# Kernel optimization log

Measured on AMD Instinct MI355X. Metric: run time of the kernel, lower is better.

The kernel has to match this reference:

```python
import jax, jax.numpy as jnp
import numpy as np

N = 100000      # nodes
E = 3200000     # edges (avg degree 32)
DIN, DH, DOUT = 128, 32, 2


def setup_inputs() -> dict:
    key = jax.random.key(0)
    k1, k2, k3, k4 = jax.random.split(key, 4)
    x = jax.random.normal(k1, (N, DIN), dtype=jnp.float32)
    edge_index = jax.random.randint(k2, (2, E), 0, N, dtype=jnp.int64)
    # Glorot-ish scaled weights
    W1 = jax.random.normal(k3, (DIN, DH), dtype=jnp.float32) / np.sqrt(DIN)
    b1 = jnp.zeros((DH,), dtype=jnp.float32)
    W2 = jax.random.normal(k4, (DH, DOUT), dtype=jnp.float32) / np.sqrt(DH)
    b2 = jnp.zeros((DOUT,), dtype=jnp.float32)
    return {"x": x, "edge_index": edge_index, "W1": W1, "b1": b1, "W2": W2, "b2": b2}


def reference(x, edge_index, W1, b1, W2, b2):
    n = x.shape[0]
    # GCNConv default: add self-loops, symmetric deg^{-1/2} A deg^{-1/2} normalization
    loops = jnp.arange(n, dtype=edge_index.dtype)
    src = jnp.concatenate([edge_index[0], loops])  # [E+N]
    dst = jnp.concatenate([edge_index[1], loops])  # [E+N]
    deg = jax.ops.segment_sum(jnp.ones_like(dst, dtype=x.dtype), dst, num_segments=n)
    dinv = jnp.where(deg > 0, jax.lax.rsqrt(deg), 0.0)
    norm = dinv[src] * dinv[dst]  # [E+N]

    def gcn_layer(h, W, b):
        m = h @ W                                   # [n, dout] transform first (PyG order)
        msgs = m[src] * norm[:, None]               # gather + scale  [E+N, dout]
        agg = jax.ops.segment_sum(msgs, dst, num_segments=n)  # scatter-add
        return agg + b

    h = jax.nn.relu(gcn_layer(x, W1, b1))
    return gcn_layer(h, W2, b2)
```

## Files before the change

### kernel.cpp

```cpp
#include <hip/hip_runtime.h>
#include <hip/hip_bf16.h>

#define DIN 128
#define DH 32
#define DOUT 2
#define NPB 128
#define NPB_SHIFT 7
#define NBUK_MAX 1024
#define FILL_EDGES 8192
#define ECHUNK 2048
#define CAP 5632

#define FXS1 2048.0f
#define FXI1 (1.0f / 2048.0f)
#define FXS2 131072.0f
#define FXI2 (1.0f / 131072.0f)


__device__ inline int sxlo(unsigned int w) { return (int)(short)(w & 0xFFFFu); }
__device__ inline int sxhi(unsigned int w) { return ((int)w) >> 16; }

__global__ void zero_kernel(int* __restrict__ gcur, int nbuk,
                            unsigned int* __restrict__ mqrow) {
    int i = blockIdx.x * blockDim.x + threadIdx.x;
    if (i < nbuk) gcur[i] = 0;
    if (blockIdx.x == 0 && threadIdx.x < 16) mqrow[threadIdx.x] = 0u;
}

__global__ void __launch_bounds__(1024, 2)
binfill_kernel(const int* __restrict__ src, const int* __restrict__ dst,
               int* __restrict__ gcur, unsigned int* __restrict__ binned,
               int e, int nbuk) {
    __shared__ int cnt[NBUK_MAX];
    __shared__ int pos[NBUK_MAX];
    __shared__ int gb[NBUK_MAX];
    __shared__ int stmp[1024];
    __shared__ unsigned int sorted[FILL_EDGES];
    __shared__ unsigned short aux[FILL_EDGES];

    int t = threadIdx.x;
    int e0 = blockIdx.x * FILL_EDGES;
    int m = min(FILL_EDGES, e - e0);

    if (t < nbuk) cnt[t] = 0;
    __syncthreads();
    for (int i = t; i < m; i += 1024) atomicAdd(&cnt[dst[e0 + i] >> NPB_SHIFT], 1);
    __syncthreads();

    int v = (t < nbuk) ? cnt[t] : 0;
    stmp[t] = v;
    __syncthreads();
    for (int off = 1; off < 1024; off <<= 1) {
        int x = (t >= off) ? stmp[t - off] : 0;
        __syncthreads();
        stmp[t] += x;
        __syncthreads();
    }
    if (t < nbuk) pos[t] = stmp[t] - v;
    __syncthreads();

    for (int i = t; i < m; i += 1024) {
        int d = dst[e0 + i];
        int sv = src[e0 + i];
        int b = d >> NPB_SHIFT;
        int r = atomicAdd(&pos[b], 1);
        sorted[r] = ((unsigned int)(d & (NPB - 1)) << 17) | (unsigned int)sv;
        aux[r] = (unsigned short)b;
    }
    __syncthreads();

    if (t < nbuk) {
        int c = cnt[t];
        gb[t] = c ? atomicAdd(&gcur[t], c) : 0;
    }
    __syncthreads();

    for (int i = t; i < m; i += 1024) {
        int b = aux[i];
        int start = pos[b] - cnt[b];
        unsigned int off = (unsigned int)(gb[b] + (i - start));
        if (off < (unsigned int)CAP)
            binned[(size_t)b * CAP + off] = sorted[i];
    }
}

__global__ void bdinv_kernel(const int* __restrict__ gcur,
                             const unsigned int* __restrict__ binned,
                             float* __restrict__ dinv, int n) {
    __shared__ int cnt[NPB];
    int t = threadIdx.x;
    int b = blockIdx.x;
    if (t < NPB) cnt[t] = 0;
    __syncthreads();
    const unsigned int* bp = binned + (size_t)b * CAP;
    const int cntb = min(gcur[b], CAP);
    for (int i = t; i < cntb; i += 256) atomicAdd(&cnt[bp[i] >> 17], 1);
    __syncthreads();
    if (t < NPB) {
        int r = (b << NPB_SHIFT) + t;
        if (r < n) dinv[r] = rsqrtf((float)(cnt[t] + 1));
    }
}

#define XTS 68
__global__ void __launch_bounds__(128, 4)
gemm1_kernel(const float* __restrict__ x, const float* __restrict__ W1,
             const float* __restrict__ dinv,
             short* __restrict__ mqc, int n) {
    __shared__ float  XT[DIN * XTS];
    __shared__ float4 Wl4[DIN * 8];

    int t = threadIdx.x;
    for (int i = t; i < DIN * 8; i += 128) Wl4[i] = ((const float4*)W1)[i];

    int rb = blockIdx.x * 64;
    for (int i = t; i < 64 * 32; i += 128) {
        int r = i & 63, kq = i >> 6;
        int gr = rb + r;
        float4 v = make_float4(0.f, 0.f, 0.f, 0.f);
        if (gr < n) v = ((const float4*)x)[(size_t)gr * 32 + kq];
        XT[(4 * kq + 0) * XTS + r] = v.x;
        XT[(4 * kq + 1) * XTS + r] = v.y;
        XT[(4 * kq + 2) * XTS + r] = v.z;
        XT[(4 * kq + 3) * XTS + r] = v.w;
    }
    __syncthreads();

    const int cq = t & 7;
    const int rq = t >> 3;
    float4 a0 = make_float4(0.f, 0.f, 0.f, 0.f);
    float4 a1 = a0, a2 = a0, a3 = a0;
#pragma unroll 8
    for (int k = 0; k < DIN; ++k) {
        float4 xv = *(const float4*)&XT[k * XTS + 4 * rq];
        float4 w  = Wl4[k * 8 + cq];
        a0.x += xv.x * w.x; a0.y += xv.x * w.y; a0.z += xv.x * w.z; a0.w += xv.x * w.w;
        a1.x += xv.y * w.x; a1.y += xv.y * w.y; a1.z += xv.y * w.z; a1.w += xv.y * w.w;
        a2.x += xv.z * w.x; a2.y += xv.z * w.y; a2.z += xv.z * w.z; a2.w += xv.z * w.w;
        a3.x += xv.w * w.x; a3.y += xv.w * w.y; a3.z += xv.w * w.z; a3.w += xv.w * w.w;
    }
#pragma unroll
    for (int m = 0; m < 4; ++m) {
        int r = rb + 4 * rq + m;
        if (r < n) {
            float di = dinv[r] * FXS1;
            float4 av = (m == 0) ? a0 : (m == 1) ? a1 : (m == 2) ? a2 : a3;
            short4 sv;
            sv.x = (short)__float2int_rn(av.x * di);
            sv.y = (short)__float2int_rn(av.y * di);
            sv.z = (short)__float2int_rn(av.z * di);
            sv.w = (short)__float2int_rn(av.w * di);
            *(short4*)&mqc[(size_t)r * DH + 4 * cq] = sv;
        }
    }
}

__global__ void __launch_bounds__(512, 8)
agg1_kernel(const int* __restrict__ gcur,
            const unsigned int* __restrict__ binned,
            const short* __restrict__ mqc,
            const float* __restrict__ dinv,
            const float* __restrict__ b1, const float* __restrict__ W2,
            float2* __restrict__ m2q, int n) {
    __shared__ int acc[NPB * 33];
    __shared__ unsigned int ebuf[2][ECHUNK];

    const int t = threadIdx.x;
    const int b = blockIdx.x;
    const int cntb = min(gcur[b], CAP);
    const int r0 = b << NPB_SHIFT;

    for (int i = t; i < NPB * 33; i += 512) acc[i] = 0;

    const unsigned int* __restrict__ bp = binned + (size_t)b * CAP;
    const unsigned int* __restrict__ mq32 = (const unsigned int*)mqc;
    const unsigned int sent = (unsigned int)n;
    const int nchunks = (cntb + ECHUNK - 1) / ECHUNK;

    unsigned int st[4];
    if (nchunks > 0) {
#pragma unroll
        for (int k = 0; k < 4; ++k) {
            int idx = t + k * 512;
            st[k] = (idx < cntb) ? __builtin_nontemporal_load(&bp[idx]) : sent;
        }
#pragma unroll
        for (int k = 0; k < 4; ++k) ebuf[0][t + k * 512] = st[k];
    }
    __syncthreads();

    const int g = t >> 4, l = t & 15;

    for (int c = 0; c < nchunks; ++c) {
        if (c + 1 < nchunks) {
            const int base = (c + 1) * ECHUNK;
#pragma unroll
            for (int k = 0; k < 4; ++k) {
                int idx = base + t + k * 512;
                st[k] = (idx < cntb) ? __builtin_nontemporal_load(&bp[idx]) : sent;
            }
        }
        const unsigned int* eb = ebuf[c & 1];
        for (int j = 0; j < 64; j += 8) {
            const unsigned int* ej = &eb[g + 32 * j];
            unsigned int e0 = ej[0],   e1 = ej[32],  e2 = ej[64],  e3 = ej[96];
            unsigned int e4 = ej[128], e5 = ej[160], e6 = ej[192], e7 = ej[224];
            unsigned int w0 = mq32[(e0 & 0x1FFFFu) * 16u + l];
            unsigned int w1 = mq32[(e1 & 0x1FFFFu) * 16u + l];
            unsigned int w2 = mq32[(e2 & 0x1FFFFu) * 16u + l];
            unsigned int w3 = mq32[(e3 & 0x1FFFFu) * 16u + l];
            unsigned int w4 = mq32[(e4 & 0x1FFFFu) * 16u + l];
            unsigned int w5 = mq32[(e5 & 0x1FFFFu) * 16u + l];
            unsigned int w6 = mq32[(e6 & 0x1FFFFu) * 16u + l];
            unsigned int w7 = mq32[(e7 & 0x1FFFFu) * 16u + l];
            int d0 = (int)(e0 >> 17) * 33 + 2 * l;
            int d1 = (int)(e1 >> 17) * 33 + 2 * l;
            int d2 = (int)(e2 >> 17) * 33 + 2 * l;
            int d3 = (int)(e3 >> 17) * 33 + 2 * l;
            int d4 = (int)(e4 >> 17) * 33 + 2 * l;
            int d5 = (int)(e5 >> 17) * 33 + 2 * l;
            int d6 = (int)(e6 >> 17) * 33 + 2 * l;
            int d7 = (int)(e7 >> 17) * 33 + 2 * l;
            atomicAdd(&acc[d0], sxlo(w0)); atomicAdd(&acc[d0 + 1], sxhi(w0));
            atomicAdd(&acc[d1], sxlo(w1)); atomicAdd(&acc[d1 + 1], sxhi(w1));
            atomicAdd(&acc[d2], sxlo(w2)); atomicAdd(&acc[d2 + 1], sxhi(w2));
            atomicAdd(&acc[d3], sxlo(w3)); atomicAdd(&acc[d3 + 1], sxhi(w3));
            atomicAdd(&acc[d4], sxlo(w4)); atomicAdd(&acc[d4 + 1], sxhi(w4));
            atomicAdd(&acc[d5], sxlo(w5)); atomicAdd(&acc[d5 + 1], sxhi(w5));
            atomicAdd(&acc[d6], sxlo(w6)); atomicAdd(&acc[d6 + 1], sxhi(w6));
            atomicAdd(&acc[d7], sxlo(w7)); atomicAdd(&acc[d7 + 1], sxhi(w7));
        }
        __syncthreads();
        if (c + 1 < nchunks) {
#pragma unroll
            for (int k = 0; k < 4; ++k) ebuf[(c + 1) & 1][t + k * 512] = st[k];
        }
        __syncthreads();
    }

    const int j = t >> 2, q = t & 3;
    const int r = r0 + j;
    if (r < n) {
        const float di = dinv[r];
        const unsigned int* srow = (const unsigned int*)mqc + (size_t)r * 16 + q * 4;
        const int* ar = &acc[j * 33 + q * 8];
        float p0 = 0.f, p1 = 0.f;
#pragma unroll
        for (int k = 0; k < 4; ++k) {
            unsigned int sw = srow[k];
            int c = q * 8 + 2 * k;
            float h0 = fmaxf(di * (float)(ar[2 * k]     + sxlo(sw)) * FXI1 + b1[c],     0.0f);
            float h1 = fmaxf(di * (float)(ar[2 * k + 1] + sxhi(sw)) * FXI1 + b1[c + 1], 0.0f);
            p0 += h0 * W2[2 * c]     + h1 * W2[2 * c + 2];
            p1 += h0 * W2[2 * c + 1] + h1 * W2[2 * c + 3];
        }
        p0 += __shfl_down(p0, 2, 4); p0 += __shfl_down(p0, 1, 4);
        p1 += __shfl_down(p1, 2, 4); p1 += __shfl_down(p1, 1, 4);
        if (q == 0) m2q[r] = make_float2(di * p0, di * p1);
    }
}

__global__ void __launch_bounds__(256, 4)
agg2_kernel(const int* __restrict__ gcur,
            const unsigned int* __restrict__ binned,
            const float2* __restrict__ m2q,
            const float* __restrict__ dinv, const float* __restrict__ b2,
            float* __restrict__ out, int n) {
    __shared__ int a0s[NPB], a1s[NPB];
    const int t = threadIdx.x;
    const int b = blockIdx.x;
    const int cntb = min(gcur[b], CAP);
    const int r0 = b << NPB_SHIFT;

    if (t < NPB) { a0s[t] = 0; a1s[t] = 0; }
    __syncthreads();

    const unsigned int* __restrict__ bp = binned + (size_t)b * CAP;
    int i = t;
    for (; i + 768 < cntb; i += 1024) {
        unsigned int e0 = __builtin_nontemporal_load(&bp[i]);
        unsigned int e1 = __builtin_nontemporal_load(&bp[i + 256]);
        unsigned int e2 = __builtin_nontemporal_load(&bp[i + 512]);
        unsigned int e3 = __builtin_nontemporal_load(&bp[i + 768]);
        float2 v0 = m2q[e0 & 0x1FFFFu];
        float2 v1 = m2q[e1 & 0x1FFFFu];
        float2 v2 = m2q[e2 & 0x1FFFFu];
        float2 v3 = m2q[e3 & 0x1FFFFu];
        atomicAdd(&a0s[e0 >> 17], __float2int_rn(v0.x * FXS2));
        atomicAdd(&a1s[e0 >> 17], __float2int_rn(v0.y * FXS2));
        atomicAdd(&a0s[e1 >> 17], __float2int_rn(v1.x * FXS2));
        atomicAdd(&a1s[e1 >> 17], __float2int_rn(v1.y * FXS2));
        atomicAdd(&a0s[e2 >> 17], __float2int_rn(v2.x * FXS2));
        atomicAdd(&a1s[e2 >> 17], __float2int_rn(v2.y * FXS2));
        atomicAdd(&a0s[e3 >> 17], __float2int_rn(v3.x * FXS2));
        atomicAdd(&a1s[e3 >> 17], __float2int_rn(v3.y * FXS2));
    }
    for (; i < cntb; i += 256) {
        unsigned int e0 = __builtin_nontemporal_load(&bp[i]);
        float2 v0 = m2q[e0 & 0x1FFFFu];
        atomicAdd(&a0s[e0 >> 17], __float2int_rn(v0.x * FXS2));
        atomicAdd(&a1s[e0 >> 17], __float2int_rn(v0.y * FXS2));
    }
    __syncthreads();

    if (t < NPB) {
        int r = r0 + t;
        if (r < n) {
            float di = dinv[r];
            float2 self = m2q[r];
            out[(size_t)r * DOUT + 0] = di * ((float)a0s[t] * FXI2 + self.x) + b2[0];
            out[(size_t)r * DOUT + 1] = di * ((float)a1s[t] * FXI2 + self.y) + b2[1];
        }
    }
}

extern "C" void kernel_launch(void* const* d_in, const int* in_sizes, int n_in,
                              void* d_out, int out_size, void* d_ws, size_t ws_size,
                              hipStream_t stream) {
    const float* x  = (const float*)d_in[0];
    const int*   ei = (const int*)d_in[1];
    const float* W1 = (const float*)d_in[2];
    const float* b1 = (const float*)d_in[3];
    const float* W2 = (const float*)d_in[4];
    const float* b2 = (const float*)d_in[5];
    float* out = (float*)d_out;

    const int n = in_sizes[0] / DIN;
    const int e = in_sizes[1] / 2;
    const int* src = ei;
    const int* dst = ei + e;
    const int nbuk = (n + NPB - 1) >> NPB_SHIFT;

    char* ws = (char*)d_ws;
    float* dinv   = (float*)ws;          ws += (size_t)n * 4;
    int* gcur     = (int*)ws;            ws += NBUK_MAX * 4;
    unsigned int* binned = (unsigned int*)ws;   ws += (size_t)nbuk * CAP * 4;
    short* mqc    = (short*)ws;          ws += ((size_t)n + 1) * DH * 2;
    float2* m2q   = (float2*)ws;

    const int B = 256;
    const int fill_blocks = (e + FILL_EDGES - 1) / FILL_EDGES;

    zero_kernel<<<(nbuk + B - 1) / B, B, 0, stream>>>(
        gcur, nbuk, (unsigned int*)(mqc + (size_t)n * DH));
    binfill_kernel<<<fill_blocks, 1024, 0, stream>>>(src, dst, gcur, binned, e, nbuk);
    bdinv_kernel<<<nbuk, B, 0, stream>>>(gcur, binned, dinv, n);
    gemm1_kernel<<<(n + 63) / 64, 128, 0, stream>>>(x, W1, dinv, mqc, n);
    agg1_kernel<<<nbuk, 512, 0, stream>>>(gcur, binned, mqc, dinv, b1, W2, m2q, n);
    agg2_kernel<<<nbuk, B, 0, stream>>>(gcur, binned, m2q, dinv, b2, out, n);
}
```

Baseline: 222.1 us.

## Split layer-1 features into two 16-channel planes and halve agg1 per block

gemm1 now writes the quantized 32-channel features as two separate 16-channel planes. agg1 launches two blocks per bucket, each gathering only one plane, so each gathered row is 32 bytes instead of 64, the shared accumulator shrinks and occupancy can rise. The blocks of a bucket are interleaved so both halves of a bucket run close together in time, which should improve L2 reuse of the per-bucket edge list that each half reads. The two halves' partial layer-2 products are combined by global integer atomics into a fixed-point m2 array that zero_kernel now clears, and agg2 consumes these integers directly. The cost is reading each edge list twice, the extra global atomics, and a larger zeroing pass.

```diff
diff --git a/kernel.cpp b/kernel.cpp
--- a/kernel.cpp
+++ b/kernel.cpp
@@ -8,7 +8,7 @@
 #define NPB_SHIFT 7
 #define NBUK_MAX 1024
 #define FILL_EDGES 8192
-#define ECHUNK 2048
+#define ECHUNK 1024
 #define CAP 5632
 
 #define FXS1 2048.0f
@@ -21,10 +21,16 @@
 __device__ inline int sxhi(unsigned int w) { return ((int)w) >> 16; }
 
 __global__ void zero_kernel(int* __restrict__ gcur, int nbuk,
-                            unsigned int* __restrict__ mqrow) {
-    int i = blockIdx.x * blockDim.x + threadIdx.x;
+                            unsigned int* __restrict__ mq32,
+                            int* __restrict__ m2qi_raw, int n) {
+    int i = blockIdx.x * 256 + threadIdx.x;
     if (i < nbuk) gcur[i] = 0;
-    if (blockIdx.x == 0 && threadIdx.x < 16) mqrow[threadIdx.x] = 0u;
+    if (i < 8) {
+        mq32[(size_t)n * 8 + i] = 0u;
+        mq32[(size_t)(n + 1) * 8 + (size_t)n * 8 + i] = 0u;
+    }
+    int total = 2 * n;
+    for (int k = i; k < total; k += gridDim.x * 256) m2qi_raw[k] = 0;
 }
 
 __global__ void __launch_bounds__(1024, 2)
@@ -139,6 +145,7 @@
         a2.x += xv.z * w.x; a2.y += xv.z * w.y; a2.z += xv.z * w.z; a2.w += xv.z * w.w;
         a3.x += xv.w * w.x; a3.y += xv.w * w.y; a3.z += xv.w * w.z; a3.w += xv.w * w.w;
     }
+    short* plane = mqc + (size_t)(cq >> 2) * ((size_t)(n + 1) * 16);
 #pragma unroll
     for (int m = 0; m < 4; ++m) {
         int r = rb + 4 * rq + m;
@@ -150,30 +157,34 @@
             sv.y = (short)__float2int_rn(av.y * di);
             sv.z = (short)__float2int_rn(av.z * di);
             sv.w = (short)__float2int_rn(av.w * di);
-            *(short4*)&mqc[(size_t)r * DH + 4 * cq] = sv;
-        }
-    }
-}
-
-__global__ void __launch_bounds__(512, 8)
+            *(short4*)&plane[(size_t)r * 16 + (cq & 3) * 4] = sv;
+        }
+    }
+}
+
+__global__ void __launch_bounds__(256, 8)
 agg1_kernel(const int* __restrict__ gcur,
             const unsigned int* __restrict__ binned,
             const short* __restrict__ mqc,
             const float* __restrict__ dinv,
             const float* __restrict__ b1, const float* __restrict__ W2,
-            float2* __restrict__ m2q, int n) {
-    __shared__ int acc[NPB * 33];
+            int* __restrict__ m2qi, int n, int nbuk) {
+    __shared__ int acc[NPB * 17];
     __shared__ unsigned int ebuf[2][ECHUNK];
 
     const int t = threadIdx.x;
-    const int b = blockIdx.x;
+    const int i8 = (int)(blockIdx.x & 7);
+    const int h  = (i8 >= 4) ? 1 : 0;
+    const int b  = (int)(blockIdx.x >> 3) * 4 + (i8 & 3);
+    if (b >= nbuk) return;
     const int cntb = min(gcur[b], CAP);
     const int r0 = b << NPB_SHIFT;
 
-    for (int i = t; i < NPB * 33; i += 512) acc[i] = 0;
+    for (int i = t; i < NPB * 17; i += 256) acc[i] = 0;
 
     const unsigned int* __restrict__ bp = binned + (size_t)b * CAP;
-    const unsigned int* __restrict__ mq32 = (const unsigned int*)mqc;
+    const unsigned int* __restrict__ mp =
+        (const unsigned int*)mqc + (size_t)h * (size_t)(n + 1) * 8;
     const unsigned int sent = (unsigned int)n;
     const int nchunks = (cntb + ECHUNK - 1) / ECHUNK;
 
@@ -181,46 +192,50 @@
     if (nchunks > 0) {
 #pragma unroll
         for (int k = 0; k < 4; ++k) {
-            int idx = t + k * 512;
+            int idx = t + k * 256;
             st[k] = (idx < cntb) ? __builtin_nontemporal_load(&bp[idx]) : sent;
         }
 #pragma unroll
-        for (int k = 0; k < 4; ++k) ebuf[0][t + k * 512] = st[k];
-    }
-    __syncthreads();
-
-    const int g = t >> 4, l = t & 15;
+        for (int k = 0; k < 4; ++k) ebuf[0][t + k * 256] = st[k];
+    }
+    __syncthreads();
+
+    const int g = t >> 4;
+    const int l = t & 15;
+    const int sub = l >> 3;
+    const int ld = l & 7;
+    const int l2 = 2 * ld;
 
     for (int c = 0; c < nchunks; ++c) {
         if (c + 1 < nchunks) {
             const int base = (c + 1) * ECHUNK;
 #pragma unroll
             for (int k = 0; k < 4; ++k) {
-                int idx = base + t + k * 512;
+                int idx = base + t + k * 256;
                 st[k] = (idx < cntb) ? __builtin_nontemporal_load(&bp[idx]) : sent;
             }
         }
         const unsigned int* eb = ebuf[c & 1];
-        for (int j = 0; j < 64; j += 8) {
-            const unsigned int* ej = &eb[g + 32 * j];
+        for (int j = 0; j < 32; j += 8) {
+            const unsigned int* ej = &eb[32 * j + 2 * g + sub];
             unsigned int e0 = ej[0],   e1 = ej[32],  e2 = ej[64],  e3 = ej[96];
             unsigned int e4 = ej[128], e5 = ej[160], e6 = ej[192], e7 = ej[224];
-            unsigned int w0 = mq32[(e0 & 0x1FFFFu) * 16u + l];
-            unsigned int w1 = mq32[(e1 & 0x1FFFFu) * 16u + l];
-            unsigned int w2 = mq32[(e2 & 0x1FFFFu) * 16u + l];
-            unsigned int w3 = mq32[(e3 & 0x1FFFFu) * 16u + l];
-            unsigned int w4 = mq32[(e4 & 0x1FFFFu) * 16u + l];
-            unsigned int w5 = mq32[(e5 & 0x1FFFFu) * 16u + l];
-            unsigned int w6 = mq32[(e6 & 0x1FFFFu) * 16u + l];
-            unsigned int w7 = mq32[(e7 & 0x1FFFFu) * 16u + l];
-            int d0 = (int)(e0 >> 17) * 33 + 2 * l;
-            int d1 = (int)(e1 >> 17) * 33 + 2 * l;
-            int d2 = (int)(e2 >> 17) * 33 + 2 * l;
-            int d3 = (int)(e3 >> 17) * 33 + 2 * l;
-            int d4 = (int)(e4 >> 17) * 33 + 2 * l;
-            int d5 = (int)(e5 >> 17) * 33 + 2 * l;
-            int d6 = (int)(e6 >> 17) * 33 + 2 * l;
-            int d7 = (int)(e7 >> 17) * 33 + 2 * l;
+            unsigned int w0 = mp[(e0 & 0x1FFFFu) * 8u + ld];
+            unsigned int w1 = mp[(e1 & 0x1FFFFu) * 8u + ld];
+            unsigned int w2 = mp[(e2 & 0x1FFFFu) * 8u + ld];
+            unsigned int w3 = mp[(e3 & 0x1FFFFu) * 8u + ld];
+            unsigned int w4 = mp[(e4 & 0x1FFFFu) * 8u + ld];
+            unsigned int w5 = mp[(e5 & 0x1FFFFu) * 8u + ld];
+            unsigned int w6 = mp[(e6 & 0x1FFFFu) * 8u + ld];
+            unsigned int w7 = mp[(e7 & 0x1FFFFu) * 8u + ld];
+            int d0 = (int)(e0 >> 17) * 17 + l2;
+            int d1 = (int)(e1 >> 17) * 17 + l2;
+            int d2 = (int)(e2 >> 17) * 17 + l2;
+            int d3 = (int)(e3 >> 17) * 17 + l2;
+            int d4 = (int)(e4 >> 17) * 17 + l2;
+            int d5 = (int)(e5 >> 17) * 17 + l2;
+            int d6 = (int)(e6 >> 17) * 17 + l2;
+            int d7 = (int)(e7 >> 17) * 17 + l2;
             atomicAdd(&acc[d0], sxlo(w0)); atomicAdd(&acc[d0 + 1], sxhi(w0));
             atomicAdd(&acc[d1], sxlo(w1)); atomicAdd(&acc[d1 + 1], sxhi(w1));
             atomicAdd(&acc[d2], sxlo(w2)); atomicAdd(&acc[d2 + 1], sxhi(w2));
@@ -233,37 +248,40 @@
         __syncthreads();
         if (c + 1 < nchunks) {
 #pragma unroll
-            for (int k = 0; k < 4; ++k) ebuf[(c + 1) & 1][t + k * 512] = st[k];
+            for (int k = 0; k < 4; ++k) ebuf[(c + 1) & 1][t + k * 256] = st[k];
         }
         __syncthreads();
     }
 
-    const int j = t >> 2, q = t & 3;
+    const int j = t >> 1, q = t & 1;
     const int r = r0 + j;
     if (r < n) {
         const float di = dinv[r];
-        const unsigned int* srow = (const unsigned int*)mqc + (size_t)r * 16 + q * 4;
-        const int* ar = &acc[j * 33 + q * 8];
+        const unsigned int* srow = mp + (size_t)r * 8 + q * 4;
+        const int* ar = &acc[j * 17 + q * 8];
         float p0 = 0.f, p1 = 0.f;
 #pragma unroll
         for (int k = 0; k < 4; ++k) {
             unsigned int sw = srow[k];
-            int c = q * 8 + 2 * k;
+            int c = h * 16 + q * 8 + 2 * k;
             float h0 = fmaxf(di * (float)(ar[2 * k]     + sxlo(sw)) * FXI1 + b1[c],     0.0f);
             float h1 = fmaxf(di * (float)(ar[2 * k + 1] + sxhi(sw)) * FXI1 + b1[c + 1], 0.0f);
             p0 += h0 * W2[2 * c]     + h1 * W2[2 * c + 2];
             p1 += h0 * W2[2 * c + 1] + h1 * W2[2 * c + 3];
         }
-        p0 += __shfl_down(p0, 2, 4); p0 += __shfl_down(p0, 1, 4);
-        p1 += __shfl_down(p1, 2, 4); p1 += __shfl_down(p1, 1, 4);
-        if (q == 0) m2q[r] = make_float2(di * p0, di * p1);
+        p0 += __shfl_down(p0, 1, 2);
+        p1 += __shfl_down(p1, 1, 2);
+        if (q == 0) {
+            atomicAdd(&m2qi[2 * r],     __float2int_rn(di * p0 * FXS2));
+            atomicAdd(&m2qi[2 * r + 1], __float2int_rn(di * p1 * FXS2));
+        }
     }
 }
 
 __global__ void __launch_bounds__(256, 4)
 agg2_kernel(const int* __restrict__ gcur,
             const unsigned int* __restrict__ binned,
-            const float2* __restrict__ m2q,
+            const int2* __restrict__ m2qi,
             const float* __restrict__ dinv, const float* __restrict__ b2,
             float* __restrict__ out, int n) {
     __shared__ int a0s[NPB], a1s[NPB];
@@ -282,24 +300,19 @@
         unsigned int e1 = __builtin_nontemporal_load(&bp[i + 256]);
         unsigned int e2 = __builtin_nontemporal_load(&bp[i + 512]);
         unsigned int e3 = __builtin_nontemporal_load(&bp[i + 768]);
-        float2 v0 = m2q[e0 & 0x1FFFFu];
-        float2 v1 = m2q[e1 & 0x1FFFFu];
-        float2 v2 = m2q[e2 & 0x1FFFFu];
-        float2 v3 = m2q[e3 & 0x1FFFFu];
-        atomicAdd(&a0s[e0 >> 17], __float2int_rn(v0.x * FXS2));
-        atomicAdd(&a1s[e0 >> 17], __float2int_rn(v0.y * FXS2));
-        atomicAdd(&a0s[e1 >> 17], __float2int_rn(v1.x * FXS2));
-        atomicAdd(&a1s[e1 >> 17], __float2int_rn(v1.y * FXS2));
-        atomicAdd(&a0s[e2 >> 17], __float2int_rn(v2.x * FXS2));
-        atomicAdd(&a1s[e2 >> 17], __float2int_rn(v2.y * FXS2));
-        atomicAdd(&a0s[e3 >> 17], __float2int_rn(v3.x * FXS2));
-        atomicAdd(&a1s[e3 >> 17], __float2int_rn(v3.y * FXS2));
+        int2 v0 = m2qi[e0 & 0x1FFFFu];
+        int2 v1 = m2qi[e1 & 0x1FFFFu];
+        int2 v2 = m2qi[e2 & 0x1FFFFu];
+        int2 v3 = m2qi[e3 & 0x1FFFFu];
+        atomicAdd(&a0s[e0 >> 17], v0.x); atomicAdd(&a1s[e0 >> 17], v0.y);
+        atomicAdd(&a0s[e1 >> 17], v1.x); atomicAdd(&a1s[e1 >> 17], v1.y);
+        atomicAdd(&a0s[e2 >> 17], v2.x); atomicAdd(&a1s[e2 >> 17], v2.y);
+        atomicAdd(&a0s[e3 >> 17], v3.x); atomicAdd(&a1s[e3 >> 17], v3.y);
     }
     for (; i < cntb; i += 256) {
         unsigned int e0 = __builtin_nontemporal_load(&bp[i]);
-        float2 v0 = m2q[e0 & 0x1FFFFu];
-        atomicAdd(&a0s[e0 >> 17], __float2int_rn(v0.x * FXS2));
-        atomicAdd(&a1s[e0 >> 17], __float2int_rn(v0.y * FXS2));
+        int2 v0 = m2qi[e0 & 0x1FFFFu];
+        atomicAdd(&a0s[e0 >> 17], v0.x); atomicAdd(&a1s[e0 >> 17], v0.y);
     }
     __syncthreads();
 
@@ -307,9 +320,9 @@
         int r = r0 + t;
         if (r < n) {
             float di = dinv[r];
-            float2 self = m2q[r];
-            out[(size_t)r * DOUT + 0] = di * ((float)a0s[t] * FXI2 + self.x) + b2[0];
-            out[(size_t)r * DOUT + 1] = di * ((float)a1s[t] * FXI2 + self.y) + b2[1];
+            int2 self = m2qi[r];
+            out[(size_t)r * DOUT + 0] = di * (float)(a0s[t] + self.x) * FXI2 + b2[0];
+            out[(size_t)r * DOUT + 1] = di * (float)(a1s[t] + self.y) * FXI2 + b2[1];
         }
     }
 }
@@ -335,17 +348,19 @@
     float* dinv   = (float*)ws;          ws += (size_t)n * 4;
     int* gcur     = (int*)ws;            ws += NBUK_MAX * 4;
     unsigned int* binned = (unsigned int*)ws;   ws += (size_t)nbuk * CAP * 4;
-    short* mqc    = (short*)ws;          ws += ((size_t)n + 1) * DH * 2;
-    float2* m2q   = (float2*)ws;
+    short* mqc    = (short*)ws;          ws += (size_t)2 * (n + 1) * 16 * 2;
+    int* m2qi     = (int*)ws;
 
     const int B = 256;
     const int fill_blocks = (e + FILL_EDGES - 1) / FILL_EDGES;
-
-    zero_kernel<<<(nbuk + B - 1) / B, B, 0, stream>>>(
-        gcur, nbuk, (unsigned int*)(mqc + (size_t)n * DH));
+    const int agg1_blocks = ((nbuk + 3) / 4) * 8;
+
+    zero_kernel<<<(2 * n + B - 1) / B, B, 0, stream>>>(
+        gcur, nbuk, (unsigned int*)mqc, m2qi, n);
     binfill_kernel<<<fill_blocks, 1024, 0, stream>>>(src, dst, gcur, binned, e, nbuk);
     bdinv_kernel<<<nbuk, B, 0, stream>>>(gcur, binned, dinv, n);
     gemm1_kernel<<<(n + 63) / 64, 128, 0, stream>>>(x, W1, dinv, mqc, n);
-    agg1_kernel<<<nbuk, 512, 0, stream>>>(gcur, binned, mqc, dinv, b1, W2, m2q, n);
-    agg2_kernel<<<nbuk, B, 0, stream>>>(gcur, binned, m2q, dinv, b2, out, n);
-}
+    agg1_kernel<<<agg1_blocks, B, 0, stream>>>(gcur, binned, mqc, dinv, b1, W2,
+                                               m2qi, n, nbuk);
+    agg2_kernel<<<nbuk, B, 0, stream>>>(gcur, binned, (const int2*)m2qi, dinv, b2, out, n);
+}
```

After: 221.9 us. Within noise of the previous version (-0.1%).
